# Kernel optimization log

Measured on AMD Instinct MI355X. Metric: run time of the kernel, lower is better.

Reference implementation:

```python
import jax, jax.numpy as jnp
import numpy as np

HEADS, DIM_HEADS = 16, 16
SCALE = DIM_HEADS ** -0.5

# (forward_perm, inverse_perm) for each axial dim of x: (B, S, E, H, W)
# axial axes are 1 (seq), 3 (H=4), 4 (W=5); emb axis 2 moved to last, axial axis to second-last
_PERMS = [
    ((0, 3, 4, 1, 2), (0, 3, 4, 1, 2)),  # seq axis (self-inverse)
    ((0, 1, 4, 3, 2), (0, 1, 4, 3, 2)),  # H axis (self-inverse)
    ((0, 1, 3, 4, 2), (0, 1, 4, 2, 3)),  # W axis
]


def _self_attn(x, wq, wkv, wo_w, wo_b):
    # x: (..., t, d); standard multi-head self-attention along t
    q = x @ wq.T                               # (..., t, 256)
    k, v = jnp.split(x @ wkv.T, 2, axis=-1)    # each (..., t, 256)
    lead, tlen = x.shape[:-2], x.shape[-2]
    sh = (*lead, tlen, HEADS, DIM_HEADS)
    q, k, v = q.reshape(sh), k.reshape(sh), v.reshape(sh)
    scores = jnp.einsum('...thd,...shd->...hts', q, k) * SCALE
    attn = jax.nn.softmax(scores, axis=-1)
    o = jnp.einsum('...hts,...shd->...thd', attn, v)
    o = o.reshape(*lead, tlen, HEADS * DIM_HEADS)
    return o @ wo_w.T + wo_b


def _axial_attention_layer(x, wq_l, wkv_l, wo_w_l, wo_b_l):
    # sum of attention along each axial dim (sum_axial_out=True)
    out = jnp.zeros_like(x)
    for a, (p, ip) in enumerate(_PERMS):
        y = jnp.transpose(x, p)
        y = _self_attn(y, wq_l[a], wkv_l[a], wo_w_l[a], wo_b_l[a])
        out = out + jnp.transpose(y, ip)
    return out


def setup_inputs() -> dict:
    key = jax.random.key(0)
    ks = jax.random.split(key, 8)
    B, S, E, H, W = 32, 64, 256, 4, 5
    return {
        'x': jax.random.normal(ks[0], (B, S, E, H, W), jnp.float32),
        'pos_s': jax.random.normal(ks[1], (1, S, E, 1, 1), jnp.float32),
        'pos_h': jax.random.normal(ks[2], (1, 1, E, H, 1), jnp.float32),
        'pos_w': jax.random.normal(ks[3], (1, 1, E, 1, W), jnp.float32),
        'wq': jax.random.normal(ks[4], (2, 3, 256, E), jnp.float32) * 0.02,
        'wkv': jax.random.normal(ks[5], (2, 3, 512, E), jnp.float32) * 0.02,
        'wo_w': jax.random.normal(ks[6], (2, 3, E, 256), jnp.float32) * 0.02,
        'wo_b': jnp.zeros((2, 3, E), jnp.float32),
        'dec_w': jax.random.normal(ks[7], (1, E), jnp.float32) * 0.02,
        'dec_b': jnp.zeros((1,), jnp.float32),
    }


def reference(x, pos_s, pos_h, pos_w, wq, wkv, wo_w, wo_b, dec_w, dec_b):
    # additive axial positional embeddings
    x = x + pos_s + pos_h + pos_w
    # two stacked AxialAttention blocks (no residual in the wrapper)
    for l in range(2):
        x = _axial_attention_layer(x, wq[l], wkv[l], wo_w[l], wo_b[l])
    # (B, S, E, H, W) -> (B, S, H, W, E), linear decode to 1 channel, sigmoid
    x = jnp.transpose(x, (0, 1, 3, 4, 2))
    return jax.nn.sigmoid(x @ dec_w.T + dec_b)
```

## Files before the change

kernel.cpp:

```cpp
#include <hip/hip_runtime.h>
#include <stdint.h>

typedef unsigned short u16;
typedef u16 u16x8 __attribute__((ext_vector_type(8)));
typedef __bf16 bf16x8 __attribute__((ext_vector_type(8)));
typedef float f32x4 __attribute__((ext_vector_type(4)));
typedef float f32x16 __attribute__((ext_vector_type(16)));

#define NE   256
#define NPOS 40960
#define QLD  1536

__device__ __forceinline__ float bf2f(u16 h) {
  union { unsigned u; float f; } c; c.u = ((unsigned)h) << 16; return c.f;
}
__device__ __forceinline__ u16 f2bf(float f) {
  union { float f; unsigned u; } c; c.f = f;
  unsigned u = c.u;
  return (u16)((u + 0x7FFFu + ((u >> 16) & 1u)) >> 16);
}
__device__ __forceinline__ unsigned pkbf(float a, float b) {
  unsigned r;
  asm("v_cvt_pk_bf16_f32 %0, %1, %2" : "=v"(r) : "v"(a), "v"(b));
  return r;
}
__device__ __forceinline__ void gll16(const void* g, void* l) {
  __builtin_amdgcn_global_load_lds(
      (const __attribute__((address_space(1))) void*)g,
      (__attribute__((address_space(3))) void*)l, 16, 0, 0);
}
template<int N> __device__ __forceinline__ void waitvm() {
  if constexpr (N == 0)       asm volatile("s_waitcnt vmcnt(0)"  ::: "memory");
  else if constexpr (N == 2)  asm volatile("s_waitcnt vmcnt(2)"  ::: "memory");
  else if constexpr (N == 4)  asm volatile("s_waitcnt vmcnt(4)"  ::: "memory");
  else if constexpr (N == 6)  asm volatile("s_waitcnt vmcnt(6)"  ::: "memory");
  else if constexpr (N == 8)  asm volatile("s_waitcnt vmcnt(8)"  ::: "memory");
  else if constexpr (N == 12) asm volatile("s_waitcnt vmcnt(12)" ::: "memory");
}

__global__ __launch_bounds__(256) void prep_kernel(
    const float* __restrict__ x, const float* __restrict__ pos_s,
    const float* __restrict__ pos_h, const float* __restrict__ pos_w,
    u16* __restrict__ xb)
{
  __shared__ float Ls[256 * 21];
  const int bs = blockIdx.x;
  const int s  = bs & 63;
  const int tid = threadIdx.x;
  const float* xp = x + (size_t)bs * 5120;
  for (int i = tid; i < 5120; i += 256) {
    int e = i / 20, hw = i % 20;
    int h = hw / 5, w = hw % 5;
    float v = xp[i] + pos_s[s * 256 + e] + pos_h[e * 4 + h] + pos_w[e * 5 + w];
    Ls[e * 21 + hw] = v;
  }
  __syncthreads();
  u16* op = xb + (size_t)bs * 20 * 256;
  for (int i = tid; i < 5120; i += 256) {
    int nl = i >> 8, e = i & 255;
    op[nl * 256 + e] = f2bf(Ls[e * 21 + nl]);
  }
}

#define PK_T1 (6*768*256)
#define PK_T2 (2*256*768)
__global__ __launch_bounds__(256) void pack_all(
    const float* __restrict__ wq, const float* __restrict__ wkv,
    const float* __restrict__ wo, const float* __restrict__ wo_b,
    u16* __restrict__ wqp, u16* __restrict__ wop, float* __restrict__ bsum)
{
  int i = blockIdx.x * 256 + threadIdx.x;
  if (i < PK_T1) {
    int la = i / (768 * 256);
    int rem = i - la * (768 * 256);
    int r = rem >> 8, c = rem & 255;
    float v = (r < 256) ? wq[(size_t)la * 65536 + r * 256 + c] * 0.25f
                        : wkv[(size_t)la * 131072 + (r - 256) * 256 + c];
    wqp[i] = f2bf(v);
  } else if (i < PK_T1 + PK_T2) {
    int j = i - PK_T1;
    int l = j / 196608;
    int rem = j - l * 196608;
    int out = rem / 768, k = rem % 768;
    int a = k >> 8, in = k & 255;
    wop[j] = f2bf(wo[(size_t)(((l * 3 + a) * 256) + out) * 256 + in]);
  } else if (i < PK_T1 + PK_T2 + 512) {
    int j = i - PK_T1 - PK_T2;
    int l = j >> 8, c = j & 255;
    bsum[j] = wo_b[(l * 3 + 0) * 256 + c] + wo_b[(l * 3 + 1) * 256 + c]
            + wo_b[(l * 3 + 2) * 256 + c];
  }
}

template<int NKT, int NBN, int TPB>
__global__ __launch_bounds__(256, 2) void gemm_stream(
    const u16* __restrict__ A, const u16* __restrict__ B,
    u16* __restrict__ Cb, int ldc)
{
  constexpr int K     = NKT * 32;
  constexpr int NSTEP = NKT * TPB;
  __shared__ alignas(16) u16 Bs[128 * K];
  __shared__ alignas(16) u16 As[2][128 * 32];

  const int nblk = gridDim.x;
  const int bid  = blockIdx.x;
  const int mapped = (bid & 7) * (nblk >> 3) + (bid >> 3);
  const int strip = mapped / NBN, bn = mapped % NBN;
  const int bm0 = strip * TPB;

  const int tid  = threadIdx.x;
  const int lane = tid & 63, w = tid >> 6;
  const int wr   = (w >> 1) * 64, wc = (w & 1) * 64;
  const int r16  = lane & 15, khi = lane >> 4;

  const u16* gB = B + (size_t)bn * 128 * K;
  const u16* gA = A + (size_t)bm0 * 128 * K;

  #pragma unroll
  for (int b = 0; b < K / 16; ++b) {
    int slot = tid + b * 256;
    int kt = slot >> 9, rem = slot & 511;
    int row = rem >> 2, c = rem & 3;
    gll16(gB + (size_t)row * K + kt * 32 + c * 8, (char*)Bs + slot * 16);
  }

  auto STAGE_A = [&](int g) {
    const int t = g / NKT, kt = g % NKT;
    const u16* tA = gA + (size_t)t * 128 * K + kt * 32;
    u16* dst = As[g & 1];
    #pragma unroll
    for (int r = 0; r < 2; ++r) {
      int i = tid + r * 256;
      int row = i >> 2, seg = (i & 3) << 3;
      gll16(tA + (size_t)row * K + seg, (char*)dst + i * 16);
    }
  };

  f32x4 acc[4][4] = {};
  STAGE_A(0);

  for (int t = 0; t < TPB; ++t) {
    #pragma unroll
    for (int kt = 0; kt < NKT; ++kt) {
      const int g = t * NKT + kt;
      __builtin_amdgcn_s_barrier();
      if (g + 1 < NSTEP) { STAGE_A(g + 1); waitvm<2>(); }
      else               { waitvm<0>(); }
      asm volatile("" ::: "memory");

      const u16* Ab = As[g & 1];
      const u16* Bk = Bs + kt * (128 * 32);
      bf16x8 af[4], bfr[4];
      #pragma unroll
      for (int m = 0; m < 4; ++m)
        af[m] = *(const bf16x8*)(Ab + (wr + m * 16 + r16) * 32 + khi * 8);
      #pragma unroll
      for (int n = 0; n < 4; ++n)
        bfr[n] = *(const bf16x8*)(Bk + (wc + n * 16 + r16) * 32 + khi * 8);
      #pragma unroll
      for (int m = 0; m < 4; ++m)
        #pragma unroll
        for (int n = 0; n < 4; ++n)
          acc[m][n] = __builtin_amdgcn_mfma_f32_16x16x32_bf16(af[m], bfr[n], acc[m][n], 0, 0, 0);
      asm volatile("" ::: "memory");
    }
    const int row0 = (bm0 + t) * 128 + wr + khi * 4;
    const int col0 = bn * 128 + wc + r16;
    #pragma unroll
    for (int m = 0; m < 4; ++m)
      #pragma unroll
      for (int n = 0; n < 4; ++n)
        #pragma unroll
        for (int j = 0; j < 4; ++j) {
          Cb[(size_t)(row0 + m * 16 + j) * ldc + col0 + n * 16] = f2bf(acc[m][n][j]);
          acc[m][n][j] = 0.f;
        }
  }
}

template<int MODE, int NKT, int NBN>
__global__ __launch_bounds__(256, 2) void gemm_bt(
    const u16* __restrict__ A, const u16* __restrict__ B,
    u16* __restrict__ Cb, const float* __restrict__ bias,
    const float* __restrict__ dw, float* __restrict__ logit,
    int ldc)
{
  constexpr int K   = NKT * 32;
  constexpr int BN  = 128;
  constexpr int NF  = BN / 32;
  constexpr int LPT = 2 + BN / 64;
  constexpr int ASZ = 128 * 32;
  constexpr int TSZ = (128 + BN) * 32;
  static_assert(NKT >= 2, "");

  __shared__ alignas(16) u16 smem[3 * TSZ];

  const int bid = blockIdx.x;
  const int cpx = gridDim.x >> 3;
  const int mapped = (bid & 7) * cpx + (bid >> 3);
  const int bm = mapped / NBN, bn = mapped % NBN;

  const int tid  = threadIdx.x;
  const int lane = tid & 63, w = tid >> 6;
  const int wr   = (w >> 1) * 64, wc = (w & 1) * (BN / 2);
  const int r16  = lane & 15, khi = lane >> 4;

  f32x4 acc[4][NF] = {};

  const u16* gA = A + (size_t)bm * 128 * K;
  const u16* gB = B + (size_t)bn * BN * K;

  auto STAGE = [&](int kt, int which) {
    u16* As = smem + which * TSZ;
    u16* Bs = As + ASZ;
    const u16* tA = gA + kt * 32;
    const u16* tB = gB + kt * 32;
    #pragma unroll
    for (int r = 0; r < 2; ++r) {
      int i = tid + r * 256;
      int row = i >> 2, seg = (i & 3) << 3;
      gll16(tA + (size_t)row * K + seg, (char*)As + i * 16);
    }
    #pragma unroll
    for (int r = 0; r < BN / 64; ++r) {
      int i = tid + r * 256;
      int row = i >> 2, seg = (i & 3) << 3;
      gll16(tB + (size_t)row * K + seg, (char*)Bs + i * 16);
    }
  };

  STAGE(0, 0);
  STAGE(1, 1);
  #pragma unroll
  for (int kt = 0; kt < NKT; ++kt) {
    const int cur = kt % 3;
    if (kt + 2 < NKT)      { STAGE(kt + 2, (kt + 2) % 3); waitvm<2 * LPT>(); }
    else if (kt + 1 < NKT) { waitvm<LPT>(); }
    else                   { waitvm<0>(); }
    __builtin_amdgcn_s_barrier();
    asm volatile("" ::: "memory");

    const u16* As = smem + cur * TSZ;
    const u16* Bs = As + ASZ;
    bf16x8 af[4], bfr[NF];
    #pragma unroll
    for (int m = 0; m < 4; ++m)
      af[m] = *(const bf16x8*)(As + (wr + m * 16 + r16) * 32 + khi * 8);
    #pragma unroll
    for (int n = 0; n < NF; ++n)
      bfr[n] = *(const bf16x8*)(Bs + (wc + n * 16 + r16) * 32 + khi * 8);
    #pragma unroll
    for (int m = 0; m < 4; ++m)
      #pragma unroll
      for (int n = 0; n < NF; ++n)
        acc[m][n] = __builtin_amdgcn_mfma_f32_16x16x32_bf16(af[m], bfr[n], acc[m][n], 0, 0, 0);

    asm volatile("" ::: "memory");
    __builtin_amdgcn_s_barrier();
  }

  const int row0 = bm * 128 + wr + khi * 4;
  const int col0 = bn * BN + wc + r16;

  if constexpr (MODE == 4) {
    float dwv[NF], bvv[NF];
    #pragma unroll
    for (int n = 0; n < NF; ++n) {
      int c = col0 + n * 16;
      dwv[n] = dw[c];
      bvv[n] = bias[c];
    }
    #pragma unroll
    for (int m = 0; m < 4; ++m) {
      #pragma unroll
      for (int j = 0; j < 4; ++j) {
        float p = 0.f;
        #pragma unroll
        for (int n = 0; n < NF; ++n) p += (acc[m][n][j] + bvv[n]) * dwv[n];
        p += __shfl_xor(p, 1);
        p += __shfl_xor(p, 2);
        p += __shfl_xor(p, 4);
        p += __shfl_xor(p, 8);
        if (r16 == 0) atomicAdd(&logit[row0 + m * 16 + j], p);
      }
    }
  } else {
    #pragma unroll
    for (int m = 0; m < 4; ++m) {
      #pragma unroll
      for (int n = 0; n < NF; ++n) {
        int c = col0 + n * 16;
        float bv = (MODE == 3) ? bias[c] : 0.f;
        #pragma unroll
        for (int j = 0; j < 4; ++j) {
          int r = row0 + m * 16 + j;
          Cb[(size_t)r * ldc + c] = f2bf(acc[m][n][j] + bv);
        }
      }
    }
  }
}

__global__ __launch_bounds__(256) void attn_seq_mfma(
    const u16* __restrict__ QKV, u16* __restrict__ Ob)
{
  const int w = threadIdx.x >> 6, lane = threadIdx.x & 63;
  const int wid = blockIdx.x * 4 + w;
  const int hd = wid & 15, g = wid >> 4;
  const int gb = g / 20, gr = g % 20;
  const int nbase = gb * 1280 + gr;
  const int lo = lane & 31, hi = lane >> 5;

  bf16x8 kf[2], qf[2];
  #pragma unroll
  for (int t = 0; t < 2; ++t) {
    size_t r = (size_t)(nbase + (lo + 32 * t) * 20) * QLD;
    kf[t] = *(const bf16x8*)(QKV + r + 256 + hd * 16 + hi * 8);
    qf[t] = *(const bf16x8*)(QKV + r +       hd * 16 + hi * 8);
  }
  union { u16 a[8]; bf16x8 v; } vt[4];
  #pragma unroll
  for (int c = 0; c < 4; ++c)
    #pragma unroll
    for (int j = 0; j < 8; ++j)
      vt[c].a[j] = QKV[(size_t)(nbase + (c * 16 + hi * 8 + j) * 20) * QLD
                       + 512 + hd * 16 + lo];

  f32x16 s00 = {}, s10 = {}, s01 = {}, s11 = {};
  s00 = __builtin_amdgcn_mfma_f32_32x32x16_bf16(kf[0], qf[0], s00, 0, 0, 0);
  s10 = __builtin_amdgcn_mfma_f32_32x32x16_bf16(kf[1], qf[0], s10, 0, 0, 0);
  s01 = __builtin_amdgcn_mfma_f32_32x32x16_bf16(kf[0], qf[1], s01, 0, 0, 0);
  s11 = __builtin_amdgcn_mfma_f32_32x32x16_bf16(kf[1], qf[1], s11, 0, 0, 0);

  auto run_qt = [&](f32x16 t0, f32x16 t1, int qt) {
    float m = -1e30f;
    #pragma unroll
    for (int r = 0; r < 16; ++r) { m = fmaxf(m, t0[r]); m = fmaxf(m, t1[r]); }
    m = fmaxf(m, __shfl_xor(m, 32));
    const float C = 1.4426950408889634f;
    float mc = m * C;
    float sum = 0.f;
    #pragma unroll
    for (int r = 0; r < 16; ++r) {
      float p0 = __builtin_amdgcn_exp2f(t0[r] * C - mc);
      float p1 = __builtin_amdgcn_exp2f(t1[r] * C - mc);
      t0[r] = p0; t1[r] = p1; sum += p0; sum += p1;
    }
    sum += __shfl_xor(sum, 32);
    float inv = __builtin_amdgcn_rcpf(sum);
    #pragma unroll
    for (int r = 0; r < 16; ++r) { t0[r] *= inv; t1[r] *= inv; }

    f32x16 oa = {};
    #pragma unroll
    for (int c = 0; c < 4; ++c) {
      const int rb = 8 * (c & 1);
      const f32x16& tt = (c < 2) ? t0 : t1;
      unsigned X0 = pkbf(tt[rb + 0], tt[rb + 1]);
      unsigned X1 = pkbf(tt[rb + 2], tt[rb + 3]);
      unsigned Y0 = pkbf(tt[rb + 4], tt[rb + 5]);
      unsigned Y1 = pkbf(tt[rb + 6], tt[rb + 7]);
      unsigned X0p = __shfl_xor((int)X0, 32), X1p = __shfl_xor((int)X1, 32);
      unsigned Y0p = __shfl_xor((int)Y0, 32), Y1p = __shfl_xor((int)Y1, 32);
      union { unsigned u[4]; bf16x8 v; } pf;
      pf.u[0] = hi ? Y0p : X0;
      pf.u[1] = hi ? Y1p : X1;
      pf.u[2] = hi ? Y0  : X0p;
      pf.u[3] = hi ? Y1  : X1p;
      oa = __builtin_amdgcn_mfma_f32_32x32x16_bf16(vt[c].v, pf.v, oa, 0, 0, 0);
    }
    unsigned P0 = pkbf(oa[0], oa[1]);
    unsigned P1 = pkbf(oa[2], oa[3]);
    unsigned P2 = pkbf(oa[4], oa[5]);
    unsigned P3 = pkbf(oa[6], oa[7]);
    unsigned sP0 = __shfl_xor((int)P0, 32), sP1 = __shfl_xor((int)P1, 32);
    unsigned sP2 = __shfl_xor((int)P2, 32), sP3 = __shfl_xor((int)P3, 32);
    union { unsigned u[4]; u16x8 v; } ov;
    ov.u[0] = hi ? sP2 : P0;
    ov.u[1] = hi ? sP3 : P1;
    ov.u[2] = hi ? P2  : sP0;
    ov.u[3] = hi ? P3  : sP1;
    u16* po = Ob + (size_t)(nbase + (qt * 32 + lo) * 20) * 768 + hd * 16 + hi * 8;
    *(u16x8*)po = ov.v;
  };
  run_qt(s00, s10, 0);
  run_qt(s01, s11, 1);
}

template<int T>
__device__ __forceinline__ void attn1(
    const u16* __restrict__ QKV, int n, int base, int stp, int hd,
    u16* __restrict__ po)
{
  const u16* qp = QKV + (size_t)n * QLD + hd * 16;
  u16x8 q0 = *(const u16x8*)(qp), q1 = *(const u16x8*)(qp + 8);
  float q[16];
  #pragma unroll
  for (int d = 0; d < 8; ++d) { q[d] = bf2f(q0[d]); q[d + 8] = bf2f(q1[d]); }

  float s[T];
  float m = -1e30f;
  #pragma unroll
  for (int j = 0; j < T; ++j) {
    const u16* kp = QKV + (size_t)(base + j * stp) * QLD + 256 + hd * 16;
    u16x8 k0 = *(const u16x8*)(kp), k1 = *(const u16x8*)(kp + 8);
    float a = 0.f;
    #pragma unroll
    for (int d = 0; d < 8; ++d) a += q[d] * bf2f(k0[d]) + q[d + 8] * bf2f(k1[d]);
    s[j] = a;
    m = fmaxf(m, a);
  }
  float sum = 0.f;
  float o[16];
  #pragma unroll
  for (int d = 0; d < 16; ++d) o[d] = 0.f;
  #pragma unroll
  for (int j = 0; j < T; ++j) {
    float pj = __expf(s[j] - m);
    sum += pj;
    const u16* vp = QKV + (size_t)(base + j * stp) * QLD + 512 + hd * 16;
    u16x8 w0 = *(const u16x8*)(vp), w1 = *(const u16x8*)(vp + 8);
    #pragma unroll
    for (int d = 0; d < 8; ++d) { o[d] += pj * bf2f(w0[d]); o[d + 8] += pj * bf2f(w1[d]); }
  }
  float inv = 1.0f / sum;
  u16x8 r0, r1;
  #pragma unroll
  for (int d = 0; d < 8; ++d) { r0[d] = f2bf(o[d] * inv); r1[d] = f2bf(o[d + 8] * inv); }
  *(u16x8*)(po)     = r0;
  *(u16x8*)(po + 8) = r1;
}

__global__ __launch_bounds__(256) void attn_hw(
    const u16* __restrict__ QKV, u16* __restrict__ Ob)
{
  const int tg = blockIdx.x * 256 + threadIdx.x;
  const int hd = tg & 15, n = tg >> 4;
  int h  = (n % 20) / 5;
  int w5 = n % 5;
  attn1<4>(QKV,       n, n - h * 5, 5, hd, Ob + (size_t)n * 768 + 256 + hd * 16);
  attn1<5>(QKV + 768, n, n - w5,    1, hd, Ob + (size_t)n * 768 + 512 + hd * 16);
}

__global__ __launch_bounds__(256) void sigmoid_kernel(
    const float* __restrict__ logit, const float* __restrict__ dec_b,
    float* __restrict__ out)
{
  int i = blockIdx.x * 256 + threadIdx.x;
  out[i] = 1.0f / (1.0f + __expf(-(logit[i] + dec_b[0])));
}

extern "C" void kernel_launch(void* const* d_in, const int* in_sizes, int n_in,
                              void* d_out, int out_size, void* d_ws, size_t ws_size,
                              hipStream_t stream) {
  const float* x     = (const float*)d_in[0];
  const float* pos_s = (const float*)d_in[1];
  const float* pos_h = (const float*)d_in[2];
  const float* pos_w = (const float*)d_in[3];
  const float* wq    = (const float*)d_in[4];
  const float* wkv   = (const float*)d_in[5];
  const float* wo_w  = (const float*)d_in[6];
  const float* wo_b  = (const float*)d_in[7];
  const float* dec_w = (const float*)d_in[8];
  const float* dec_b = (const float*)d_in[9];
  float* out = (float*)d_out;

  char* ws = (char*)d_ws;
  u16*   xb    = (u16*)ws;
  u16*   Ob    = (u16*)(ws + 20971520);
  u16*   QKV   = (u16*)(ws + 83886080);
  u16*   wqp   = (u16*)(ws + 209715200);
  u16*   wop   = (u16*)(ws + 212074496);
  float* bsum  = (float*)(ws + 212860928);
  float* logit = (float*)(ws + 212862976);

  prep_kernel<<<2048, 256, 0, stream>>>(x, pos_s, pos_h, pos_w, xb);
  pack_all<<<(PK_T1 + PK_T2 + 512 + 255) / 256, 256, 0, stream>>>(
      wq, wkv, wo_w, wo_b, wqp, wop, bsum);
  hipMemsetAsync(logit, 0, NPOS * sizeof(float), stream);

  for (int l = 0; l < 2; ++l) {
    gemm_stream<8, 6, 4><<<480, 256, 0, stream>>>(
        xb, wqp + (size_t)(l * 3) * 196608, QKV, QLD);
    attn_seq_mfma<<<2560, 256, 0, stream>>>(QKV, Ob);
    gemm_stream<8, 12, 4><<<960, 256, 0, stream>>>(
        xb, wqp + (size_t)(l * 3 + 1) * 196608, QKV, QLD);
    attn_hw<<<2560, 256, 0, stream>>>(QKV, Ob);
    if (l == 0)
      gemm_bt<3, 24, 2><<<320 * 2, 256, 0, stream>>>(
          Ob, wop, xb, bsum, nullptr, nullptr, 256);
    else
      gemm_bt<4, 24, 2><<<320 * 2, 256, 0, stream>>>(
          Ob, wop + 196608, nullptr, bsum + 256, dec_w, logit, 0);
  }

  sigmoid_kernel<<<NPOS / 256, 256, 0, stream>>>(logit, dec_b, out);
}
```

Baseline: 335.2 us.

## Merge QKV projections into one GEMM, write attention in place, swizzle LDS

The two QKV projection GEMM launches become a single wider GEMM that writes all three axial QKV blocks into one buffer with row stride 2304. The attention kernels now overwrite each Q slot with their output, which removes the separate Ob buffer and its traffic. The output GEMM gathers A columns from those strided Q slots. LDS tiles in both GEMMs use an XOR swizzle on the 16-byte segment index to cut bank conflicts on fragment reads. The price is a larger QKV buffer and more complex A addressing in the output GEMM.

```diff
diff --git a/kernel.cpp b/kernel.cpp
--- a/kernel.cpp
+++ b/kernel.cpp
@@ -9,7 +9,7 @@
 
 #define NE   256
 #define NPOS 40960
-#define QLD  1536
+#define QLD  2304
 
 __device__ __forceinline__ float bf2f(u16 h) {
   union { unsigned u; float f; } c; c.u = ((unsigned)h) << 16; return c.f;
@@ -33,9 +33,7 @@
   if constexpr (N == 0)       asm volatile("s_waitcnt vmcnt(0)"  ::: "memory");
   else if constexpr (N == 2)  asm volatile("s_waitcnt vmcnt(2)"  ::: "memory");
   else if constexpr (N == 4)  asm volatile("s_waitcnt vmcnt(4)"  ::: "memory");
-  else if constexpr (N == 6)  asm volatile("s_waitcnt vmcnt(6)"  ::: "memory");
   else if constexpr (N == 8)  asm volatile("s_waitcnt vmcnt(8)"  ::: "memory");
-  else if constexpr (N == 12) asm volatile("s_waitcnt vmcnt(12)" ::: "memory");
 }
 
 __global__ __launch_bounds__(256) void prep_kernel(
@@ -112,6 +110,7 @@
   const int lane = tid & 63, w = tid >> 6;
   const int wr   = (w >> 1) * 64, wc = (w & 1) * 64;
   const int r16  = lane & 15, khi = lane >> 4;
+  const int pofs = (khi ^ ((r16 >> 1) & 3)) * 8;
 
   const u16* gB = B + (size_t)bn * 128 * K;
   const u16* gA = A + (size_t)bm0 * 128 * K;
@@ -121,7 +120,8 @@
     int slot = tid + b * 256;
     int kt = slot >> 9, rem = slot & 511;
     int row = rem >> 2, c = rem & 3;
-    gll16(gB + (size_t)row * K + kt * 32 + c * 8, (char*)Bs + slot * 16);
+    int cs = c ^ ((row >> 1) & 3);
+    gll16(gB + (size_t)row * K + kt * 32 + cs * 8, (char*)Bs + slot * 16);
   }
 
   auto STAGE_A = [&](int g) {
@@ -131,8 +131,9 @@
     #pragma unroll
     for (int r = 0; r < 2; ++r) {
       int i = tid + r * 256;
-      int row = i >> 2, seg = (i & 3) << 3;
-      gll16(tA + (size_t)row * K + seg, (char*)dst + i * 16);
+      int row = i >> 2, s = i & 3;
+      int ss = s ^ ((row >> 1) & 3);
+      gll16(tA + (size_t)row * K + ss * 8, (char*)dst + i * 16);
     }
   };
 
@@ -153,10 +154,10 @@
       bf16x8 af[4], bfr[4];
       #pragma unroll
       for (int m = 0; m < 4; ++m)
-        af[m] = *(const bf16x8*)(Ab + (wr + m * 16 + r16) * 32 + khi * 8);
+        af[m] = *(const bf16x8*)(Ab + (wr + m * 16 + r16) * 32 + pofs);
       #pragma unroll
       for (int n = 0; n < 4; ++n)
-        bfr[n] = *(const bf16x8*)(Bk + (wc + n * 16 + r16) * 32 + khi * 8);
+        bfr[n] = *(const bf16x8*)(Bk + (wc + n * 16 + r16) * 32 + pofs);
       #pragma unroll
       for (int m = 0; m < 4; ++m)
         #pragma unroll
@@ -186,13 +187,7 @@
     int ldc)
 {
   constexpr int K   = NKT * 32;
-  constexpr int BN  = 128;
-  constexpr int NF  = BN / 32;
-  constexpr int LPT = 2 + BN / 64;
-  constexpr int ASZ = 128 * 32;
-  constexpr int TSZ = (128 + BN) * 32;
-  static_assert(NKT >= 2, "");
-
+  constexpr int TSZ = 256 * 32;
   __shared__ alignas(16) u16 smem[3 * TSZ];
 
   const int bid = blockIdx.x;
@@ -202,30 +197,32 @@
 
   const int tid  = threadIdx.x;
   const int lane = tid & 63, w = tid >> 6;
-  const int wr   = (w >> 1) * 64, wc = (w & 1) * (BN / 2);
+  const int wr   = (w >> 1) * 64, wc = (w & 1) * 64;
   const int r16  = lane & 15, khi = lane >> 4;
-
-  f32x4 acc[4][NF] = {};
-
-  const u16* gA = A + (size_t)bm * 128 * K;
-  const u16* gB = B + (size_t)bn * BN * K;
+  const int pofs = (khi ^ ((r16 >> 1) & 3)) * 8;
+
+  f32x4 acc[4][4] = {};
+
+  const u16* gA = A + (size_t)bm * 128 * QLD;
+  const u16* gB = B + (size_t)bn * 128 * K;
 
   auto STAGE = [&](int kt, int which) {
     u16* As = smem + which * TSZ;
-    u16* Bs = As + ASZ;
-    const u16* tA = gA + kt * 32;
-    const u16* tB = gB + kt * 32;
+    u16* Bsl = As + 128 * 32;
     #pragma unroll
     for (int r = 0; r < 2; ++r) {
       int i = tid + r * 256;
-      int row = i >> 2, seg = (i & 3) << 3;
-      gll16(tA + (size_t)row * K + seg, (char*)As + i * 16);
-    }
-    #pragma unroll
-    for (int r = 0; r < BN / 64; ++r) {
+      int row = i >> 2, s = i & 3;
+      int col = kt * 32 + (s ^ ((row >> 1) & 3)) * 8;
+      int phys = (col >> 8) * 768 + (col & 255);
+      gll16(gA + (size_t)row * QLD + phys, (char*)As + i * 16);
+    }
+    #pragma unroll
+    for (int r = 0; r < 2; ++r) {
       int i = tid + r * 256;
-      int row = i >> 2, seg = (i & 3) << 3;
-      gll16(tB + (size_t)row * K + seg, (char*)Bs + i * 16);
+      int row = i >> 2, s = i & 3;
+      int ss = s ^ ((row >> 1) & 3);
+      gll16(gB + (size_t)row * K + kt * 32 + ss * 8, (char*)Bsl + i * 16);
     }
   };
 
@@ -234,25 +231,25 @@
   #pragma unroll
   for (int kt = 0; kt < NKT; ++kt) {
     const int cur = kt % 3;
-    if (kt + 2 < NKT)      { STAGE(kt + 2, (kt + 2) % 3); waitvm<2 * LPT>(); }
-    else if (kt + 1 < NKT) { waitvm<LPT>(); }
+    if (kt + 2 < NKT)      { STAGE(kt + 2, (kt + 2) % 3); waitvm<8>(); }
+    else if (kt + 1 < NKT) { waitvm<4>(); }
     else                   { waitvm<0>(); }
     __builtin_amdgcn_s_barrier();
     asm volatile("" ::: "memory");
 
     const u16* As = smem + cur * TSZ;
-    const u16* Bs = As + ASZ;
-    bf16x8 af[4], bfr[NF];
+    const u16* Bsl = As + 128 * 32;
+    bf16x8 af[4], bfr[4];
     #pragma unroll
     for (int m = 0; m < 4; ++m)
-      af[m] = *(const bf16x8*)(As + (wr + m * 16 + r16) * 32 + khi * 8);
-    #pragma unroll
-    for (int n = 0; n < NF; ++n)
-      bfr[n] = *(const bf16x8*)(Bs + (wc + n * 16 + r16) * 32 + khi * 8);
+      af[m] = *(const bf16x8*)(As + (wr + m * 16 + r16) * 32 + pofs);
+    #pragma unroll
+    for (int n = 0; n < 4; ++n)
+      bfr[n] = *(const bf16x8*)(Bsl + (wc + n * 16 + r16) * 32 + pofs);
     #pragma unroll
     for (int m = 0; m < 4; ++m)
       #pragma unroll
-      for (int n = 0; n < NF; ++n)
+      for (int n = 0; n < 4; ++n)
         acc[m][n] = __builtin_amdgcn_mfma_f32_16x16x32_bf16(af[m], bfr[n], acc[m][n], 0, 0, 0);
 
     asm volatile("" ::: "memory");
@@ -260,12 +257,12 @@
   }
 
   const int row0 = bm * 128 + wr + khi * 4;
-  const int col0 = bn * BN + wc + r16;
+  const int col0 = bn * 128 + wc + r16;
 
   if constexpr (MODE == 4) {
-    float dwv[NF], bvv[NF];
-    #pragma unroll
-    for (int n = 0; n < NF; ++n) {
+    float dwv[4], bvv[4];
+    #pragma unroll
+    for (int n = 0; n < 4; ++n) {
       int c = col0 + n * 16;
       dwv[n] = dw[c];
       bvv[n] = bias[c];
@@ -276,7 +273,7 @@
       for (int j = 0; j < 4; ++j) {
         float p = 0.f;
         #pragma unroll
-        for (int n = 0; n < NF; ++n) p += (acc[m][n][j] + bvv[n]) * dwv[n];
+        for (int n = 0; n < 4; ++n) p += (acc[m][n][j] + bvv[n]) * dwv[n];
         p += __shfl_xor(p, 1);
         p += __shfl_xor(p, 2);
         p += __shfl_xor(p, 4);
@@ -288,9 +285,9 @@
     #pragma unroll
     for (int m = 0; m < 4; ++m) {
       #pragma unroll
-      for (int n = 0; n < NF; ++n) {
+      for (int n = 0; n < 4; ++n) {
         int c = col0 + n * 16;
-        float bv = (MODE == 3) ? bias[c] : 0.f;
+        float bv = bias[c];
         #pragma unroll
         for (int j = 0; j < 4; ++j) {
           int r = row0 + m * 16 + j;
@@ -301,8 +298,7 @@
   }
 }
 
-__global__ __launch_bounds__(256) void attn_seq_mfma(
-    const u16* __restrict__ QKV, u16* __restrict__ Ob)
+__global__ __launch_bounds__(256) void attn_seq_mfma(u16* __restrict__ QKV)
 {
   const int w = threadIdx.x >> 6, lane = threadIdx.x & 63;
   const int wid = blockIdx.x * 4 + w;
@@ -380,7 +376,7 @@
     ov.u[1] = hi ? sP3 : P1;
     ov.u[2] = hi ? P2  : sP0;
     ov.u[3] = hi ? P3  : sP1;
-    u16* po = Ob + (size_t)(nbase + (qt * 32 + lo) * 20) * 768 + hd * 16 + hi * 8;
+    u16* po = QKV + (size_t)(nbase + (qt * 32 + lo) * 20) * QLD + hd * 16 + hi * 8;
     *(u16x8*)po = ov.v;
   };
   run_qt(s00, s10, 0);
@@ -389,10 +385,9 @@
 
 template<int T>
 __device__ __forceinline__ void attn1(
-    const u16* __restrict__ QKV, int n, int base, int stp, int hd,
-    u16* __restrict__ po)
-{
-  const u16* qp = QKV + (size_t)n * QLD + hd * 16;
+    u16* __restrict__ Qb, int n, int base, int stp, int hd)
+{
+  u16* qp = Qb + (size_t)n * QLD + hd * 16;
   u16x8 q0 = *(const u16x8*)(qp), q1 = *(const u16x8*)(qp + 8);
   float q[16];
   #pragma unroll
@@ -402,7 +397,7 @@
   float m = -1e30f;
   #pragma unroll
   for (int j = 0; j < T; ++j) {
-    const u16* kp = QKV + (size_t)(base + j * stp) * QLD + 256 + hd * 16;
+    const u16* kp = Qb + (size_t)(base + j * stp) * QLD + 256 + hd * 16;
     u16x8 k0 = *(const u16x8*)(kp), k1 = *(const u16x8*)(kp + 8);
     float a = 0.f;
     #pragma unroll
@@ -418,7 +413,7 @@
   for (int j = 0; j < T; ++j) {
     float pj = __expf(s[j] - m);
     sum += pj;
-    const u16* vp = QKV + (size_t)(base + j * stp) * QLD + 512 + hd * 16;
+    const u16* vp = Qb + (size_t)(base + j * stp) * QLD + 512 + hd * 16;
     u16x8 w0 = *(const u16x8*)(vp), w1 = *(const u16x8*)(vp + 8);
     #pragma unroll
     for (int d = 0; d < 8; ++d) { o[d] += pj * bf2f(w0[d]); o[d + 8] += pj * bf2f(w1[d]); }
@@ -427,19 +422,18 @@
   u16x8 r0, r1;
   #pragma unroll
   for (int d = 0; d < 8; ++d) { r0[d] = f2bf(o[d] * inv); r1[d] = f2bf(o[d + 8] * inv); }
-  *(u16x8*)(po)     = r0;
-  *(u16x8*)(po + 8) = r1;
-}
-
-__global__ __launch_bounds__(256) void attn_hw(
-    const u16* __restrict__ QKV, u16* __restrict__ Ob)
+  *(u16x8*)(qp)     = r0;
+  *(u16x8*)(qp + 8) = r1;
+}
+
+__global__ __launch_bounds__(256) void attn_hw(u16* __restrict__ QKV)
 {
   const int tg = blockIdx.x * 256 + threadIdx.x;
   const int hd = tg & 15, n = tg >> 4;
   int h  = (n % 20) / 5;
   int w5 = n % 5;
-  attn1<4>(QKV,       n, n - h * 5, 5, hd, Ob + (size_t)n * 768 + 256 + hd * 16);
-  attn1<5>(QKV + 768, n, n - w5,    1, hd, Ob + (size_t)n * 768 + 512 + hd * 16);
+  attn1<4>(QKV + 768,  n, n - h * 5, 5, hd);
+  attn1<5>(QKV + 1536, n, n - w5,    1, hd);
 }
 
 __global__ __launch_bounds__(256) void sigmoid_kernel(
@@ -467,8 +461,7 @@
 
   char* ws = (char*)d_ws;
   u16*   xb    = (u16*)ws;
-  u16*   Ob    = (u16*)(ws + 20971520);
-  u16*   QKV   = (u16*)(ws + 83886080);
+  u16*   QKV   = (u16*)(ws + 20971520);
   u16*   wqp   = (u16*)(ws + 209715200);
   u16*   wop   = (u16*)(ws + 212074496);
   float* bsum  = (float*)(ws + 212860928);
@@ -480,18 +473,16 @@
   hipMemsetAsync(logit, 0, NPOS * sizeof(float), stream);
 
   for (int l = 0; l < 2; ++l) {
-    gemm_stream<8, 6, 4><<<480, 256, 0, stream>>>(
+    gemm_stream<8, 18, 4><<<1440, 256, 0, stream>>>(
         xb, wqp + (size_t)(l * 3) * 196608, QKV, QLD);
-    attn_seq_mfma<<<2560, 256, 0, stream>>>(QKV, Ob);
-    gemm_stream<8, 12, 4><<<960, 256, 0, stream>>>(
-        xb, wqp + (size_t)(l * 3 + 1) * 196608, QKV, QLD);
-    attn_hw<<<2560, 256, 0, stream>>>(QKV, Ob);
+    attn_seq_mfma<<<2560, 256, 0, stream>>>(QKV);
+    attn_hw<<<2560, 256, 0, stream>>>(QKV);
     if (l == 0)
-      gemm_bt<3, 24, 2><<<320 * 2, 256, 0, stream>>>(
-          Ob, wop, xb, bsum, nullptr, nullptr, 256);
+      gemm_bt<3, 24, 2><<<640, 256, 0, stream>>>(
+          QKV, wop, xb, bsum, nullptr, nullptr, 256);
     else
-      gemm_bt<4, 24, 2><<<320 * 2, 256, 0, stream>>>(
-          Ob, wop + 196608, nullptr, bsum + 256, dec_w, logit, 0);
+      gemm_bt<4, 24, 2><<<640, 256, 0, stream>>>(
+          QKV, wop + 196608, nullptr, bsum + 256, dec_w, logit, 0);
   }
 
   sigmoid_kernel<<<NPOS / 256, 256, 0, stream>>>(logit, dec_b, out);
```

Measured after the change: 324.2 us. -3.3%, faster.
